# Performance work log

Measured on AMD Instinct MI355X. Metric: run time of the kernel, lower is better.

## Reference

```python
import jax, jax.numpy as jnp
import numpy as np

B, L, D = 8, 4096, 512  # batch, seq_len (power of 2), in_features
R_MIN, R_MAX = 0.9, 0.999


def setup_inputs() -> dict:
    key = jax.random.key(0)
    k1, k2, k3 = jax.random.split(key, 3)
    inputs = jax.random.normal(k1, (B, L, D), dtype=jnp.float32)
    # Linear layers: i_dense D->2D, o_dense 2D->D (torch Linear: y = x @ W.T + b)
    Wi = jax.random.normal(k2, (2 * D, D), dtype=jnp.float32) / np.sqrt(D)
    bi = jnp.zeros((2 * D,), dtype=jnp.float32)
    Wo = jax.random.normal(k3, (D, 2 * D), dtype=jnp.float32) / np.sqrt(2 * D)
    bo = jnp.zeros((D,), dtype=jnp.float32)
    # LRU param init, exactly as in the torch module
    rng = np.random.RandomState(0)
    u1 = rng.random_sample(D)
    u2 = rng.random_sample(D)
    v_log = np.log(-0.5 * np.log(u1 * (R_MAX ** 2 - R_MIN ** 2) + R_MIN ** 2))
    theta_log = np.log(u2 * np.pi * 2)
    gamma_log = np.log(np.sqrt(1 - np.exp(-np.exp(v_log)) ** 2))
    params_log = jnp.asarray(np.stack([v_log, theta_log, gamma_log]), dtype=jnp.float32)
    return {"inputs": inputs, "Wi": Wi, "bi": bi, "Wo": Wo, "bo": bo,
            "params_log": params_log}


def reference(inputs, Wi, bi, Wo, bo, params_log):
    b, lin, d = inputs.shape
    u = inputs @ Wi.T + bi                       # [B, L, 2D]
    params = jnp.exp(params_log)                 # [3, D]
    v, theta, gamma = params[0], params[1], params[2]
    log2_L = int(np.ceil(np.log2(lin)))
    Lp = 2 ** log2_L
    # interleaved (real, imag) pairs -> complex state
    u = u.reshape(b, lin, d, 2)
    x = jax.lax.complex(u[..., 0], u[..., 1])    # [B, L, D] complex64
    if Lp > lin:
        x = jnp.pad(x, ((0, 0), (0, Lp - lin), (0, 0)))
    # Blelloch-style doubling scan: after stage i, each block of length 2^i
    # holds the prefix-scanned values x_t = lam*x_{t-1} + u_t within the block.
    for i in range(1, log2_L + 1):
        l = 2 ** i
        xr = x.reshape(b * Lp // l, l, d)
        x1, x2 = xr[:, : l // 2], xr[:, l // 2 :]
        pos = jnp.arange(1, l // 2 + 1, dtype=jnp.float32)        # [l/2]
        lambs = jnp.exp(jax.lax.complex(-pos[:, None] * v,
                                        pos[:, None] * theta))   # [l/2, D]
        x2 = x2 + lambs * x1[:, -1:]
        x = jnp.concatenate([x1, x2], axis=1).reshape(b, Lp, d)
    x = x[:, :lin] * gamma.astype(jnp.complex64)
    xr = jnp.concatenate([jnp.real(x), jnp.imag(x)], axis=-1)     # [B, L, 2D]
    out = xr @ Wo.T + bo
    return jax.nn.relu(out)
```

## Files before the change

kernel.cpp:

```cpp
#include <hip/hip_runtime.h>
#include <cstdint>
#include <cstddef>

typedef unsigned short u16;
typedef unsigned int   u32;

typedef short bf16x8 __attribute__((ext_vector_type(8)));
typedef float f32x4  __attribute__((ext_vector_type(4)));

__device__ __forceinline__ u16 f2bf(float f) {
  u32 u = __float_as_uint(f);
  u += 0x7fffu + ((u >> 16) & 1u);
  return (u16)(u >> 16);
}
__device__ __forceinline__ float bflo(u32 w) { return __uint_as_float((w & 0xffffu) << 16); }
__device__ __forceinline__ float bfhi(u32 w) { return __uint_as_float(w & 0xffff0000u); }

#define GLB_AS(p) ((const __attribute__((address_space(1))) void*)(p))
#define LDS_AS(p) ((__attribute__((address_space(3))) void*)(p))

__global__ __launch_bounds__(256)
void conv3_f32_bf16(const float* __restrict__ in, u16* __restrict__ a,
                    const float* __restrict__ wi, u16* __restrict__ wib,
                    const float* __restrict__ wo, u16* __restrict__ wob)
{
  long i = (long)blockIdx.x * 256 + threadIdx.x;
  const float* src; u16* dst;
  if (i < 4194304L) { src = in; dst = a; }
  else if (i < 4325376L) { i -= 4194304L; src = wi; dst = wib; }
  else { i -= 4325376L; if (i >= 131072L) return; src = wo; dst = wob; }
  float4 v = ((const float4*)src)[i];
  u32 lo = (u32)f2bf(v.x) | ((u32)f2bf(v.y) << 16);
  u32 hi = (u32)f2bf(v.z) | ((u32)f2bf(v.w) << 16);
  ((uint2*)dst)[i] = make_uint2(lo, hi);
}

template<int N, int K, int LOGNB, int OUT_BF16, int RELU>
__global__ __launch_bounds__(512, 4)
void gemm_w2(const u16* __restrict__ A, const u16* __restrict__ Bw,
             const float* __restrict__ bias, void* __restrict__ Cout)
{
  __shared__ __align__(16) u16 As[256 * 32];
  __shared__ __align__(16) u16 Bs[128 * 32];

  const int tid  = threadIdx.x;
  const int lane = tid & 63;
  const int wave = tid >> 6;
  const int bid  = blockIdx.x;
  const int xcd  = bid & 7;
  const int s    = bid >> 3;
  const int m0 = (xcd * 16 + (s >> LOGNB)) * 256;
  const int n0 = (s & ((1 << LOGNB) - 1)) * 128;
  const int wm = (wave & 3) * 64;
  const int wn = (wave >> 2) * 64;

  f32x4 acc[4][4];
#pragma unroll
  for (int i = 0; i < 4; ++i)
#pragma unroll
    for (int j = 0; j < 4; ++j) acc[i][j] = f32x4{0.f, 0.f, 0.f, 0.f};

  const u16* Ap[2]; const u16* Bp; int ldsA[2]; int ldsB;
#pragma unroll
  for (int i = 0; i < 2; ++i) {
    int g = i * 512 + tid;
    int r = g >> 2;
    int koff = ((g & 3) ^ ((r >> 1) & 3)) << 3;
    Ap[i]   = A + (size_t)(m0 + r) * K + koff;
    ldsA[i] = (i * 512 + wave * 64) * 8;
  }
  {
    int g = tid;
    int r = g >> 2;
    int koff = ((g & 3) ^ ((r >> 1) & 3)) << 3;
    Bp   = Bw + (size_t)(n0 + r) * K + koff;
    ldsB = (wave * 64) * 8;
  }

  const int fm = lane & 15;
  const int q  = lane >> 4;
  int aoff[4], boff[4];
#pragma unroll
  for (int i = 0; i < 4; ++i) {
    int m = wm + i * 16 + fm;
    aoff[i] = (m * 4 + (q ^ ((m >> 1) & 3))) * 8;
    int n = wn + i * 16 + fm;
    boff[i] = (n * 4 + (q ^ ((n >> 1) & 3))) * 8;
  }

  for (int kt = 0; kt < K; kt += 32) {
    __builtin_amdgcn_global_load_lds(GLB_AS(Ap[0] + kt), LDS_AS(As + ldsA[0]), 16, 0, 0);
    __builtin_amdgcn_global_load_lds(GLB_AS(Ap[1] + kt), LDS_AS(As + ldsA[1]), 16, 0, 0);
    __builtin_amdgcn_global_load_lds(GLB_AS(Bp    + kt), LDS_AS(Bs + ldsB),    16, 0, 0);
    __syncthreads();

    bf16x8 af[4], bf[4];
#pragma unroll
    for (int i = 0; i < 4; ++i) { af[i] = *(const bf16x8*)&As[aoff[i]];
                                  bf[i] = *(const bf16x8*)&Bs[boff[i]]; }
#pragma unroll
    for (int mi = 0; mi < 4; ++mi)
#pragma unroll
      for (int ni = 0; ni < 4; ++ni)
        acc[mi][ni] = __builtin_amdgcn_mfma_f32_16x16x32_bf16(af[mi], bf[ni],
                                                              acc[mi][ni], 0, 0, 0);
    __syncthreads();
  }

  const int colL = lane & 15;
  const int rowQ = (lane >> 4) * 4;
#pragma unroll
  for (int mi = 0; mi < 4; ++mi) {
#pragma unroll
    for (int ni = 0; ni < 4; ++ni) {
      int col  = n0 + wn + ni * 16 + colL;
      int rowb = m0 + wm + mi * 16 + rowQ;
      float bv = bias[col];
#pragma unroll
      for (int r = 0; r < 4; ++r) {
        float v = acc[mi][ni][r] + bv;
        if (RELU) v = fmaxf(v, 0.f);
        size_t idx = (size_t)(rowb + r) * N + col;
        if (OUT_BF16) ((u16*)Cout)[idx] = f2bf(v);
        else          ((float*)Cout)[idx] = v;
      }
    }
  }
}

__global__ __launch_bounds__(512)
void scan_chunk_end(const u16* __restrict__ u, const float* __restrict__ plog,
                    float2* __restrict__ e)
{
  const int j = threadIdx.x;
  const int c = blockIdx.x;
  const int b = blockIdx.y;
  float vv  = expf(plog[j]);
  float th  = expf(plog[512 + j]);
  float mag = expf(-vv);
  float lr = mag * cosf(th), li = mag * sinf(th);
  const u32* up = (const u32*)u;
  size_t idx = (size_t)(b * 4096 + c * 128) * 512 + j;
  float hr = 0.f, hi = 0.f;
#pragma unroll 8
  for (int t = 0; t < 128; ++t) {
    u32 w = up[idx]; idx += 512;
    float ur = bflo(w), ui = bfhi(w);
    float nr = fmaf(lr, hr, fmaf(-li, hi, ur));
    float ni2 = fmaf(lr, hi, fmaf(li, hr, ui));
    hr = nr; hi = ni2;
  }
  e[(size_t)(b * 32 + c) * 512 + j] = make_float2(hr, hi);
}

__global__ __launch_bounds__(512)
void scan_out2(const u16* __restrict__ u, const float* __restrict__ plog,
               const float2* __restrict__ e, u16* __restrict__ xr)
{
  const int j = threadIdx.x;
  const int c = blockIdx.x;
  const int b = blockIdx.y;
  float vv  = expf(plog[j]);
  float th  = expf(plog[512 + j]);
  float gm  = expf(plog[1024 + j]);
  float mag = expf(-vv);
  float lr = mag * cosf(th), li = mag * sinf(th);

  float Lm = expf(-128.f * vv);
  float La = 128.f * th;
  float Lr = Lm * cosf(La), Li = Lm * sinf(La);
  float hr = 0.f, hi = 0.f;
  for (int i = 0; i < c; ++i) {
    float2 ec = e[(size_t)(b * 32 + i) * 512 + j];
    float nr = fmaf(Lr, hr, fmaf(-Li, hi, ec.x));
    float ni2 = fmaf(Lr, hi, fmaf(Li, hr, ec.y));
    hr = nr; hi = ni2;
  }

  const u32* up = (const u32*)u;
  size_t uidx = (size_t)(b * 4096 + c * 128) * 512 + j;
  size_t xidx = (size_t)(b * 4096 + c * 128) * 1024 + j;
#pragma unroll 4
  for (int t = 0; t < 128; ++t) {
    u32 w = up[uidx]; uidx += 512;
    float ur = bflo(w), ui = bfhi(w);
    float nr = fmaf(lr, hr, fmaf(-li, hi, ur));
    float ni2 = fmaf(lr, hi, fmaf(li, hr, ui));
    hr = nr; hi = ni2;
    xr[xidx]       = f2bf(gm * hr);
    xr[xidx + 512] = f2bf(gm * hi);
    xidx += 1024;
  }
}

extern "C" void kernel_launch(void* const* d_in, const int* in_sizes, int n_in,
                              void* d_out, int out_size, void* d_ws, size_t ws_size,
                              hipStream_t stream)
{
  (void)in_sizes; (void)n_in; (void)out_size; (void)ws_size;
  const float* inputs = (const float*)d_in[0];
  const float* Wi     = (const float*)d_in[1];
  const float* bi     = (const float*)d_in[2];
  const float* Wo     = (const float*)d_in[3];
  const float* bo     = (const float*)d_in[4];
  const float* plog   = (const float*)d_in[5];

  char* ws = (char*)d_ws;
  u16*    xrA   = (u16*)(ws);
  u16*    u_bf  = (u16*)(ws + 67108864ull);
  u16*    Wi_bf = (u16*)(ws + 134217728ull);
  u16*    Wo_bf = (u16*)(ws + 135266304ull);
  float2* e_b   = (float2*)(ws + 136314880ull);

  conv3_f32_bf16<<<17408, 256, 0, stream>>>(inputs, xrA, Wi, Wi_bf, Wo, Wo_bf);

  gemm_w2<1024, 512, 3, 1, 0><<<1024, 512, 0, stream>>>(xrA, Wi_bf, bi, u_bf);

  scan_chunk_end<<<dim3(32, 8), 512, 0, stream>>>(u_bf, plog, e_b);
  scan_out2<<<dim3(32, 8), 512, 0, stream>>>(u_bf, plog, e_b, xrA);

  gemm_w2<512, 1024, 2, 0, 1><<<512, 512, 0, stream>>>(xrA, Wo_bf, bo, d_out);
}
```

Baseline: 258.1 us.

## Split scan into smaller chunks, two channels per thread with vectorized loads/stores

The chunked linear-recurrence scan now uses 128 chunks of 32 timesteps instead of 32 chunks of 128, with 256 threads each handling two adjacent channels. Loads become 8-byte uint2 reads, and the outputs pack two bf16 values into 32-bit stores instead of 16-bit scattered writes. The aim is to fill more CUs with blocks (1024 vs 256), cut the serial per-thread chain length, and improve memory coalescing. In exchange, the carry-propagation loop over previous chunk ends grows to up to 127 steps, and more chunk-end data is written and read.

```diff
diff --git a/kernel.cpp b/kernel.cpp
--- a/kernel.cpp
+++ b/kernel.cpp
@@ -128,68 +128,84 @@
   }
 }
 
-__global__ __launch_bounds__(512)
+__global__ __launch_bounds__(256)
 void scan_chunk_end(const u16* __restrict__ u, const float* __restrict__ plog,
                     float2* __restrict__ e)
 {
-  const int j = threadIdx.x;
+  const int t = threadIdx.x;
   const int c = blockIdx.x;
   const int b = blockIdx.y;
-  float vv  = expf(plog[j]);
-  float th  = expf(plog[512 + j]);
-  float mag = expf(-vv);
-  float lr = mag * cosf(th), li = mag * sinf(th);
-  const u32* up = (const u32*)u;
-  size_t idx = (size_t)(b * 4096 + c * 128) * 512 + j;
-  float hr = 0.f, hi = 0.f;
+  const int j0 = 2 * t;
+  float v0 = expf(plog[j0]),        v1 = expf(plog[j0 + 1]);
+  float t0 = expf(plog[512 + j0]),  t1 = expf(plog[512 + j0 + 1]);
+  float m0 = expf(-v0), m1 = expf(-v1);
+  float lr0 = m0 * cosf(t0), li0 = m0 * sinf(t0);
+  float lr1 = m1 * cosf(t1), li1 = m1 * sinf(t1);
+  const uint2* up = (const uint2*)u;
+  size_t idx = (size_t)(b * 4096 + c * 32) * 256 + t;
+  float h0r = 0.f, h0i = 0.f, h1r = 0.f, h1i = 0.f;
 #pragma unroll 8
-  for (int t = 0; t < 128; ++t) {
-    u32 w = up[idx]; idx += 512;
-    float ur = bflo(w), ui = bfhi(w);
-    float nr = fmaf(lr, hr, fmaf(-li, hi, ur));
-    float ni2 = fmaf(lr, hi, fmaf(li, hr, ui));
-    hr = nr; hi = ni2;
-  }
-  e[(size_t)(b * 32 + c) * 512 + j] = make_float2(hr, hi);
-}
-
-__global__ __launch_bounds__(512)
+  for (int s = 0; s < 32; ++s) {
+    uint2 w = up[idx]; idx += 256;
+    float u0r = bflo(w.x), u0i = bfhi(w.x);
+    float u1r = bflo(w.y), u1i = bfhi(w.y);
+    float n0r = fmaf(lr0, h0r, fmaf(-li0, h0i, u0r));
+    float n0i = fmaf(lr0, h0i, fmaf( li0, h0r, u0i));
+    float n1r = fmaf(lr1, h1r, fmaf(-li1, h1i, u1r));
+    float n1i = fmaf(lr1, h1i, fmaf( li1, h1r, u1i));
+    h0r = n0r; h0i = n0i; h1r = n1r; h1i = n1i;
+  }
+  ((float4*)e)[(size_t)(b * 128 + c) * 256 + t] = make_float4(h0r, h0i, h1r, h1i);
+}
+
+__global__ __launch_bounds__(256)
 void scan_out2(const u16* __restrict__ u, const float* __restrict__ plog,
                const float2* __restrict__ e, u16* __restrict__ xr)
 {
-  const int j = threadIdx.x;
+  const int t = threadIdx.x;
   const int c = blockIdx.x;
   const int b = blockIdx.y;
-  float vv  = expf(plog[j]);
-  float th  = expf(plog[512 + j]);
-  float gm  = expf(plog[1024 + j]);
-  float mag = expf(-vv);
-  float lr = mag * cosf(th), li = mag * sinf(th);
-
-  float Lm = expf(-128.f * vv);
-  float La = 128.f * th;
-  float Lr = Lm * cosf(La), Li = Lm * sinf(La);
-  float hr = 0.f, hi = 0.f;
+  const int j0 = 2 * t;
+  float v0 = expf(plog[j0]),        v1 = expf(plog[j0 + 1]);
+  float t0 = expf(plog[512 + j0]),  t1 = expf(plog[512 + j0 + 1]);
+  float g0 = expf(plog[1024 + j0]), g1 = expf(plog[1024 + j0 + 1]);
+  float m0 = expf(-v0), m1 = expf(-v1);
+  float lr0 = m0 * cosf(t0), li0 = m0 * sinf(t0);
+  float lr1 = m1 * cosf(t1), li1 = m1 * sinf(t1);
+
+  float Lm0 = expf(-32.f * v0), Lm1 = expf(-32.f * v1);
+  float La0 = 32.f * t0,        La1 = 32.f * t1;
+  float Lr0 = Lm0 * cosf(La0), Li0 = Lm0 * sinf(La0);
+  float Lr1 = Lm1 * cosf(La1), Li1 = Lm1 * sinf(La1);
+  float h0r = 0.f, h0i = 0.f, h1r = 0.f, h1i = 0.f;
+  const float4* e4 = (const float4*)e;
+#pragma unroll 4
   for (int i = 0; i < c; ++i) {
-    float2 ec = e[(size_t)(b * 32 + i) * 512 + j];
-    float nr = fmaf(Lr, hr, fmaf(-Li, hi, ec.x));
-    float ni2 = fmaf(Lr, hi, fmaf(Li, hr, ec.y));
-    hr = nr; hi = ni2;
-  }
-
-  const u32* up = (const u32*)u;
-  size_t uidx = (size_t)(b * 4096 + c * 128) * 512 + j;
-  size_t xidx = (size_t)(b * 4096 + c * 128) * 1024 + j;
-#pragma unroll 4
-  for (int t = 0; t < 128; ++t) {
-    u32 w = up[uidx]; uidx += 512;
-    float ur = bflo(w), ui = bfhi(w);
-    float nr = fmaf(lr, hr, fmaf(-li, hi, ur));
-    float ni2 = fmaf(lr, hi, fmaf(li, hr, ui));
-    hr = nr; hi = ni2;
-    xr[xidx]       = f2bf(gm * hr);
-    xr[xidx + 512] = f2bf(gm * hi);
-    xidx += 1024;
+    float4 ec = e4[(size_t)(b * 128 + i) * 256 + t];
+    float n0r = fmaf(Lr0, h0r, fmaf(-Li0, h0i, ec.x));
+    float n0i = fmaf(Lr0, h0i, fmaf( Li0, h0r, ec.y));
+    float n1r = fmaf(Lr1, h1r, fmaf(-Li1, h1i, ec.z));
+    float n1i = fmaf(Lr1, h1i, fmaf( Li1, h1r, ec.w));
+    h0r = n0r; h0i = n0i; h1r = n1r; h1i = n1i;
+  }
+
+  const uint2* up = (const uint2*)u;
+  u32* xp = (u32*)xr;
+  size_t uidx = (size_t)(b * 4096 + c * 32) * 256 + t;
+  size_t xidx = (size_t)(b * 4096 + c * 32) * 512 + t;
+#pragma unroll 8
+  for (int s = 0; s < 32; ++s) {
+    uint2 w = up[uidx]; uidx += 256;
+    float u0r = bflo(w.x), u0i = bfhi(w.x);
+    float u1r = bflo(w.y), u1i = bfhi(w.y);
+    float n0r = fmaf(lr0, h0r, fmaf(-li0, h0i, u0r));
+    float n0i = fmaf(lr0, h0i, fmaf( li0, h0r, u0i));
+    float n1r = fmaf(lr1, h1r, fmaf(-li1, h1i, u1r));
+    float n1i = fmaf(lr1, h1i, fmaf( li1, h1r, u1i));
+    h0r = n0r; h0i = n0i; h1r = n1r; h1i = n1i;
+    xp[xidx]       = (u32)f2bf(g0 * h0r) | ((u32)f2bf(g1 * h1r) << 16);
+    xp[xidx + 256] = (u32)f2bf(g0 * h0i) | ((u32)f2bf(g1 * h1i) << 16);
+    xidx += 512;
   }
 }
 
@@ -216,8 +232,8 @@
 
   gemm_w2<1024, 512, 3, 1, 0><<<1024, 512, 0, stream>>>(xrA, Wi_bf, bi, u_bf);
 
-  scan_chunk_end<<<dim3(32, 8), 512, 0, stream>>>(u_bf, plog, e_b);
-  scan_out2<<<dim3(32, 8), 512, 0, stream>>>(u_bf, plog, e_b, xrA);
+  scan_chunk_end<<<dim3(128, 8), 256, 0, stream>>>(u_bf, plog, e_b);
+  scan_out2<<<dim3(128, 8), 256, 0, stream>>>(u_bf, plog, e_b, xrA);
 
   gemm_w2<512, 1024, 2, 0, 1><<<512, 512, 0, stream>>>(xrA, Wo_bf, bo, d_out);
 }
```

Result: no change. 258.6 us (+0.2%).

## Double-buffer GEMM LDS tiles and restructure scan into smaller vectorized chunks

Applied to the files above, without the earlier changes.

The GEMM now double-buffers its LDS tiles. The next k-tile's global-to-LDS load is issued before computing the current one, with one barrier per iteration instead of two. The scan kernels now use 128 chunks of 32 steps instead of 32 chunks of 128. Each thread handles 4 channels with 16-byte loads and packed 8-byte stores, which gives more parallelism and wider memory accesses. The costs are a longer sequential carry loop over up to 127 chunk ends and doubled LDS per GEMM block, which may reduce occupancy.

```diff
diff --git a/kernel.cpp b/kernel.cpp
--- a/kernel.cpp
+++ b/kernel.cpp
@@ -40,8 +40,8 @@
 void gemm_w2(const u16* __restrict__ A, const u16* __restrict__ Bw,
              const float* __restrict__ bias, void* __restrict__ Cout)
 {
-  __shared__ __align__(16) u16 As[256 * 32];
-  __shared__ __align__(16) u16 Bs[128 * 32];
+  __shared__ __align__(16) u16 As[2][256 * 32];
+  __shared__ __align__(16) u16 Bs[2][128 * 32];
 
   const int tid  = threadIdx.x;
   const int lane = tid & 63;
@@ -88,24 +88,35 @@
     boff[i] = (n * 4 + (q ^ ((n >> 1) & 3))) * 8;
   }
 
-  for (int kt = 0; kt < K; kt += 32) {
-    __builtin_amdgcn_global_load_lds(GLB_AS(Ap[0] + kt), LDS_AS(As + ldsA[0]), 16, 0, 0);
-    __builtin_amdgcn_global_load_lds(GLB_AS(Ap[1] + kt), LDS_AS(As + ldsA[1]), 16, 0, 0);
-    __builtin_amdgcn_global_load_lds(GLB_AS(Bp    + kt), LDS_AS(Bs + ldsB),    16, 0, 0);
+  auto stage = [&](int buf, int kt) {
+    __builtin_amdgcn_global_load_lds(GLB_AS(Ap[0] + kt), LDS_AS(&As[buf][ldsA[0]]), 16, 0, 0);
+    __builtin_amdgcn_global_load_lds(GLB_AS(Ap[1] + kt), LDS_AS(&As[buf][ldsA[1]]), 16, 0, 0);
+    __builtin_amdgcn_global_load_lds(GLB_AS(Bp    + kt), LDS_AS(&Bs[buf][ldsB]),    16, 0, 0);
+  };
+  auto compute = [&](int buf) {
+    bf16x8 af[4], bfr[4];
+#pragma unroll
+    for (int i = 0; i < 4; ++i) { af[i]  = *(const bf16x8*)&As[buf][aoff[i]];
+                                  bfr[i] = *(const bf16x8*)&Bs[buf][boff[i]]; }
+#pragma unroll
+    for (int mi = 0; mi < 4; ++mi)
+#pragma unroll
+      for (int ni = 0; ni < 4; ++ni)
+        acc[mi][ni] = __builtin_amdgcn_mfma_f32_16x16x32_bf16(af[mi], bfr[ni],
+                                                              acc[mi][ni], 0, 0, 0);
+  };
+
+  constexpr int NT = K / 32;
+  stage(0, 0);
+  __syncthreads();
+  int cur = 0;
+  for (int t = 0; t < NT - 1; ++t) {
+    stage(cur ^ 1, (t + 1) * 32);
+    compute(cur);
     __syncthreads();
-
-    bf16x8 af[4], bf[4];
-#pragma unroll
-    for (int i = 0; i < 4; ++i) { af[i] = *(const bf16x8*)&As[aoff[i]];
-                                  bf[i] = *(const bf16x8*)&Bs[boff[i]]; }
-#pragma unroll
-    for (int mi = 0; mi < 4; ++mi)
-#pragma unroll
-      for (int ni = 0; ni < 4; ++ni)
-        acc[mi][ni] = __builtin_amdgcn_mfma_f32_16x16x32_bf16(af[mi], bf[ni],
-                                                              acc[mi][ni], 0, 0, 0);
-    __syncthreads();
-  }
+    cur ^= 1;
+  }
+  compute(cur);
 
   const int colL = lane & 15;
   const int rowQ = (lane >> 4) * 4;
@@ -128,68 +139,113 @@
   }
 }
 
-__global__ __launch_bounds__(512)
+__global__ __launch_bounds__(256)
 void scan_chunk_end(const u16* __restrict__ u, const float* __restrict__ plog,
-                    float2* __restrict__ e)
-{
-  const int j = threadIdx.x;
-  const int c = blockIdx.x;
-  const int b = blockIdx.y;
-  float vv  = expf(plog[j]);
-  float th  = expf(plog[512 + j]);
-  float mag = expf(-vv);
-  float lr = mag * cosf(th), li = mag * sinf(th);
-  const u32* up = (const u32*)u;
-  size_t idx = (size_t)(b * 4096 + c * 128) * 512 + j;
-  float hr = 0.f, hi = 0.f;
+                    float4* __restrict__ e)
+{
+  const int t  = threadIdx.x;
+  const int tt = t & 127;
+  const int c  = blockIdx.x * 2 + (t >> 7);
+  const int b  = blockIdx.y;
+  float4 vl = ((const float4*)plog)[tt];
+  float4 tl = ((const float4*)plog)[128 + tt];
+  float vlog[4] = {vl.x, vl.y, vl.z, vl.w};
+  float tlog[4] = {tl.x, tl.y, tl.z, tl.w};
+  float lr[4], li[4], hr[4], hi4[4];
+#pragma unroll
+  for (int k = 0; k < 4; ++k) {
+    float v  = expf(vlog[k]);
+    float th = expf(tlog[k]);
+    float mg = expf(-v);
+    lr[k] = mg * cosf(th); li[k] = mg * sinf(th);
+    hr[k] = 0.f; hi4[k] = 0.f;
+  }
+  const uint4* up = (const uint4*)u;
+  size_t idx = (size_t)(b * 4096 + c * 32) * 128 + tt;
 #pragma unroll 8
-  for (int t = 0; t < 128; ++t) {
-    u32 w = up[idx]; idx += 512;
-    float ur = bflo(w), ui = bfhi(w);
-    float nr = fmaf(lr, hr, fmaf(-li, hi, ur));
-    float ni2 = fmaf(lr, hi, fmaf(li, hr, ui));
-    hr = nr; hi = ni2;
-  }
-  e[(size_t)(b * 32 + c) * 512 + j] = make_float2(hr, hi);
-}
-
-__global__ __launch_bounds__(512)
+  for (int s = 0; s < 32; ++s) {
+    uint4 w = up[idx]; idx += 128;
+    u32 ws[4] = {w.x, w.y, w.z, w.w};
+#pragma unroll
+    for (int k = 0; k < 4; ++k) {
+      float ur = bflo(ws[k]), ui = bfhi(ws[k]);
+      float nr = fmaf(lr[k], hr[k], fmaf(-li[k], hi4[k], ur));
+      float ni = fmaf(lr[k], hi4[k], fmaf( li[k], hr[k], ui));
+      hr[k] = nr; hi4[k] = ni;
+    }
+  }
+  size_t eb = (size_t)(b * 128 + c) * 256 + 2 * tt;
+  e[eb]     = make_float4(hr[0], hi4[0], hr[1], hi4[1]);
+  e[eb + 1] = make_float4(hr[2], hi4[2], hr[3], hi4[3]);
+}
+
+__global__ __launch_bounds__(256)
 void scan_out2(const u16* __restrict__ u, const float* __restrict__ plog,
-               const float2* __restrict__ e, u16* __restrict__ xr)
-{
-  const int j = threadIdx.x;
-  const int c = blockIdx.x;
-  const int b = blockIdx.y;
-  float vv  = expf(plog[j]);
-  float th  = expf(plog[512 + j]);
-  float gm  = expf(plog[1024 + j]);
-  float mag = expf(-vv);
-  float lr = mag * cosf(th), li = mag * sinf(th);
-
-  float Lm = expf(-128.f * vv);
-  float La = 128.f * th;
-  float Lr = Lm * cosf(La), Li = Lm * sinf(La);
-  float hr = 0.f, hi = 0.f;
+               const float4* __restrict__ e, u16* __restrict__ xr)
+{
+  const int t  = threadIdx.x;
+  const int tt = t & 127;
+  const int c  = blockIdx.x * 2 + (t >> 7);
+  const int b  = blockIdx.y;
+  float4 vl = ((const float4*)plog)[tt];
+  float4 tl = ((const float4*)plog)[128 + tt];
+  float4 gl = ((const float4*)plog)[256 + tt];
+  float vlog[4] = {vl.x, vl.y, vl.z, vl.w};
+  float tlog[4] = {tl.x, tl.y, tl.z, tl.w};
+  float glog[4] = {gl.x, gl.y, gl.z, gl.w};
+  float lr[4], li[4], Lr[4], Li[4], gm[4], hr[4], hi4[4];
+#pragma unroll
+  for (int k = 0; k < 4; ++k) {
+    float v  = expf(vlog[k]);
+    float th = expf(tlog[k]);
+    gm[k] = expf(glog[k]);
+    float mg = expf(-v);
+    lr[k] = mg * cosf(th); li[k] = mg * sinf(th);
+    float Lm = expf(-32.f * v);
+    float La = 32.f * th;
+    Lr[k] = Lm * cosf(La); Li[k] = Lm * sinf(La);
+    hr[k] = 0.f; hi4[k] = 0.f;
+  }
+
+  size_t ebase = (size_t)(b * 128) * 256 + 2 * tt;
+#pragma unroll 4
   for (int i = 0; i < c; ++i) {
-    float2 ec = e[(size_t)(b * 32 + i) * 512 + j];
-    float nr = fmaf(Lr, hr, fmaf(-Li, hi, ec.x));
-    float ni2 = fmaf(Lr, hi, fmaf(Li, hr, ec.y));
-    hr = nr; hi = ni2;
-  }
-
-  const u32* up = (const u32*)u;
-  size_t uidx = (size_t)(b * 4096 + c * 128) * 512 + j;
-  size_t xidx = (size_t)(b * 4096 + c * 128) * 1024 + j;
-#pragma unroll 4
-  for (int t = 0; t < 128; ++t) {
-    u32 w = up[uidx]; uidx += 512;
-    float ur = bflo(w), ui = bfhi(w);
-    float nr = fmaf(lr, hr, fmaf(-li, hi, ur));
-    float ni2 = fmaf(lr, hi, fmaf(li, hr, ui));
-    hr = nr; hi = ni2;
-    xr[xidx]       = f2bf(gm * hr);
-    xr[xidx + 512] = f2bf(gm * hi);
-    xidx += 1024;
+    float4 e0 = e[ebase + (size_t)i * 256];
+    float4 e1 = e[ebase + (size_t)i * 256 + 1];
+    float n0r = fmaf(Lr[0], hr[0], fmaf(-Li[0], hi4[0], e0.x));
+    float n0i = fmaf(Lr[0], hi4[0], fmaf( Li[0], hr[0], e0.y));
+    float n1r = fmaf(Lr[1], hr[1], fmaf(-Li[1], hi4[1], e0.z));
+    float n1i = fmaf(Lr[1], hi4[1], fmaf( Li[1], hr[1], e0.w));
+    float n2r = fmaf(Lr[2], hr[2], fmaf(-Li[2], hi4[2], e1.x));
+    float n2i = fmaf(Lr[2], hi4[2], fmaf( Li[2], hr[2], e1.y));
+    float n3r = fmaf(Lr[3], hr[3], fmaf(-Li[3], hi4[3], e1.z));
+    float n3i = fmaf(Lr[3], hi4[3], fmaf( Li[3], hr[3], e1.w));
+    hr[0] = n0r; hi4[0] = n0i; hr[1] = n1r; hi4[1] = n1i;
+    hr[2] = n2r; hi4[2] = n2i; hr[3] = n3r; hi4[3] = n3i;
+  }
+
+  const uint4* up = (const uint4*)u;
+  uint2* xp = (uint2*)xr;
+  size_t uidx = (size_t)(b * 4096 + c * 32) * 128 + tt;
+  size_t xidx = (size_t)(b * 4096 + c * 32) * 256 + tt;
+#pragma unroll 8
+  for (int s2 = 0; s2 < 32; ++s2) {
+    uint4 w = up[uidx]; uidx += 128;
+    u32 ws[4] = {w.x, w.y, w.z, w.w};
+#pragma unroll
+    for (int k = 0; k < 4; ++k) {
+      float ur = bflo(ws[k]), ui = bfhi(ws[k]);
+      float nr = fmaf(lr[k], hr[k], fmaf(-li[k], hi4[k], ur));
+      float ni = fmaf(lr[k], hi4[k], fmaf( li[k], hr[k], ui));
+      hr[k] = nr; hi4[k] = ni;
+    }
+    u32 re0 = (u32)f2bf(gm[0] * hr[0])  | ((u32)f2bf(gm[1] * hr[1])  << 16);
+    u32 re1 = (u32)f2bf(gm[2] * hr[2])  | ((u32)f2bf(gm[3] * hr[3])  << 16);
+    u32 im0 = (u32)f2bf(gm[0] * hi4[0]) | ((u32)f2bf(gm[1] * hi4[1]) << 16);
+    u32 im1 = (u32)f2bf(gm[2] * hi4[2]) | ((u32)f2bf(gm[3] * hi4[3]) << 16);
+    xp[xidx]       = make_uint2(re0, re1);
+    xp[xidx + 128] = make_uint2(im0, im1);
+    xidx += 256;
   }
 }
 
@@ -210,14 +266,14 @@
   u16*    u_bf  = (u16*)(ws + 67108864ull);
   u16*    Wi_bf = (u16*)(ws + 134217728ull);
   u16*    Wo_bf = (u16*)(ws + 135266304ull);
-  float2* e_b   = (float2*)(ws + 136314880ull);
+  float4* e_b   = (float4*)(ws + 136314880ull);
 
   conv3_f32_bf16<<<17408, 256, 0, stream>>>(inputs, xrA, Wi, Wi_bf, Wo, Wo_bf);
 
   gemm_w2<1024, 512, 3, 1, 0><<<1024, 512, 0, stream>>>(xrA, Wi_bf, bi, u_bf);
 
-  scan_chunk_end<<<dim3(32, 8), 512, 0, stream>>>(u_bf, plog, e_b);
-  scan_out2<<<dim3(32, 8), 512, 0, stream>>>(u_bf, plog, e_b, xrA);
+  scan_chunk_end<<<dim3(64, 8), 256, 0, stream>>>(u_bf, plog, e_b);
+  scan_out2<<<dim3(64, 8), 256, 0, stream>>>(u_bf, plog, e_b, xrA);
 
   gemm_w2<512, 1024, 2, 0, 1><<<512, 512, 0, stream>>>(xrA, Wo_bf, bo, d_out);
 }
```

Result: no change. 254.7 us (-1.3%).
